# Kernel optimization log

Hardware: AMD Instinct MI355X
Metric: run time of the kernel (lower is better)

## Reference

```python
import jax, jax.numpy as jnp
import numpy as np

B, N, D, L = 8, 2048, 256, 2  # batch, node_size, in_dim==mem_dim, num_layers


def setup_inputs() -> dict:
    key = jax.random.key(0)
    k_nodes, k_adj, k_w0, k_b0, k_wr, k_br = jax.random.split(key, 6)
    nodes = jax.random.normal(k_nodes, (B, N, D), dtype=jnp.float32)
    adj = jax.random.uniform(k_adj, (B, N, N), dtype=jnp.float32)
    s = 1.0 / np.sqrt(D)
    W0_w = jax.random.uniform(k_w0, (L, D, D), dtype=jnp.float32, minval=-s, maxval=s)
    W0_b = jax.random.uniform(k_b0, (L, D), dtype=jnp.float32, minval=-s, maxval=s)
    Wr_w = jax.random.uniform(k_wr, (L, D, D), dtype=jnp.float32, minval=-s, maxval=s)
    Wr_b = jax.random.uniform(k_br, (L, D), dtype=jnp.float32, minval=-s, maxval=s)
    return {"nodes": nodes, "adj": adj, "W0_w": W0_w, "W0_b": W0_b,
            "Wr_w": Wr_w, "Wr_b": Wr_b}


def reference(nodes, adj, W0_w, W0_b, Wr_w, Wr_b):
    # denom[b] = row-sum of adj[b] + 1  -> [B, N, 1]
    denom = jnp.sum(adj, axis=2, keepdims=True) + 1.0
    x = nodes  # dropout is identity in eval mode
    outputs = x
    for l in range(L):
        # W_r branch: aggregate neighbor-transformed features
        xWr = jnp.einsum('bnd,md->bnm', x, Wr_w[l]) + Wr_b[l]   # [B,N,D]
        AxW = jnp.einsum('bnk,bkd->bnd', adj, xWr)              # sparse mm equiv
        # W_0 self branch, fused norm + relu
        xW0 = jnp.einsum('bnd,md->bnm', x, W0_w[l]) + W0_b[l]
        x = jax.nn.relu((AxW + xW0) / denom)
    return outputs + x
```

## Files before the change

### kernel.cpp

```cpp
#include <hip/hip_runtime.h>

constexpr int B = 8;
constexpr int N = 2048;
constexpr int D = 256;
constexpr int L = 2;
constexpr int M = B * N;

typedef __bf16 bf16x8 __attribute__((ext_vector_type(8)));
typedef float  f32x4  __attribute__((ext_vector_type(4)));

static __device__ __forceinline__ unsigned short f2bf(float f) {
    union { float f; unsigned u; } v; v.f = f;
    unsigned r = v.u + 0x7fffu + ((v.u >> 16) & 1u);
    return (unsigned short)(r >> 16);
}

static __device__ __forceinline__ float bf2f(unsigned short u) {
    union { unsigned u; float f; } v; v.u = ((unsigned)u) << 16;
    return v.f;
}

static __device__ __forceinline__ void gload16(const void* g, void* l) {
    __builtin_amdgcn_global_load_lds(
        (__attribute__((address_space(1))) void*)(g),
        (__attribute__((address_space(3))) void*)(l),
        16, 0, 0);
}

__global__ __launch_bounds__(256)
void denom_cast_kernel(const float* __restrict__ adj,
                       unsigned short* __restrict__ adjb,
                       float* __restrict__ rdenom,
                       float* __restrict__ rowsum) {
    const int wave = threadIdx.x >> 6;
    const int lane = threadIdx.x & 63;
    const int row  = blockIdx.x * 4 + wave;
    const float4* p = (const float4*)(adj + (size_t)row * N);
    ushort4* q = (ushort4*)(adjb + (size_t)row * N);
    float s = 0.f;
    #pragma unroll
    for (int i = 0; i < 8; ++i) {
        float4 v = p[lane + i * 64];
        s += (v.x + v.y) + (v.z + v.w);
        ushort4 o;
        o.x = f2bf(v.x); o.y = f2bf(v.y); o.z = f2bf(v.z); o.w = f2bf(v.w);
        q[lane + i * 64] = o;
    }
    #pragma unroll
    for (int off = 32; off > 0; off >>= 1) s += __shfl_down(s, off);
    if (lane == 0) {
        rowsum[row] = s;
        rdenom[row] = 1.0f / (s + 1.0f);
    }
}

__global__ __launch_bounds__(256)
void cast_nodes_kernel(const float* __restrict__ nodes,
                       unsigned short* __restrict__ nodesbf,
                       unsigned short* __restrict__ nodesT) {
    __shared__ unsigned short T[64][68];
    const int b  = blockIdx.z;
    const int n0 = blockIdx.y * 64;
    const int d0 = blockIdx.x * 64;
    const int t  = threadIdx.x;
    const int r  = t >> 2;
    const int c4 = t & 3;
    const float*    src = nodes   + ((size_t)b * N + n0) * D + d0;
    unsigned short* dst = nodesbf + ((size_t)b * N + n0) * D + d0;
    #pragma unroll
    for (int rep = 0; rep < 4; ++rep) {
        const int fc = c4 + rep * 4;
        float4 v = *(const float4*)(src + (size_t)r * D + fc * 4);
        ushort4 o;
        o.x = f2bf(v.x); o.y = f2bf(v.y); o.z = f2bf(v.z); o.w = f2bf(v.w);
        *(ushort4*)(dst + (size_t)r * D + fc * 4) = o;
        *(ushort4*)&T[r][fc * 4] = o;
    }
    __syncthreads();
    unsigned short* dstT = nodesT + ((size_t)b * D + d0) * N + n0;
    #pragma unroll
    for (int rep = 0; rep < 4; ++rep) {
        const int nc = c4 + rep * 4;
        ushort4 o;
        o.x = T[nc * 4 + 0][r];
        o.y = T[nc * 4 + 1][r];
        o.z = T[nc * 4 + 2][r];
        o.w = T[nc * 4 + 3][r];
        *(ushort4*)(dstT + (size_t)r * N + nc * 4) = o;
    }
}

__global__ __launch_bounds__(256)
void cast_w_kernel(const float* __restrict__ W0_w, const float* __restrict__ Wr_w,
                   unsigned short* __restrict__ W0b, unsigned short* __restrict__ Wrb) {
    const int i = blockIdx.x * 256 + threadIdx.x;
    float4 a = ((const float4*)W0_w)[i];
    ushort4 o0; o0.x = f2bf(a.x); o0.y = f2bf(a.y); o0.z = f2bf(a.z); o0.w = f2bf(a.w);
    ((ushort4*)W0b)[i] = o0;
    float4 c = ((const float4*)Wr_w)[i];
    ushort4 o1; o1.x = f2bf(c.x); o1.y = f2bf(c.y); o1.z = f2bf(c.z); o1.w = f2bf(c.w);
    ((ushort4*)Wrb)[i] = o1;
}

__global__ __launch_bounds__(256)
void big_mfma_kernel(const unsigned short* __restrict__ adjb,
                     const unsigned short* __restrict__ xT,
                     unsigned short* __restrict__ ypart) {
    __shared__ unsigned short As[16 * 512];
    __shared__ unsigned short Bs[16 * 512];

    const int z     = blockIdx.z;
    const int b     = z & 7;
    const int split = z >> 3;
    const int n0    = blockIdx.x * 128;
    const int m0    = blockIdx.y * 128;
    const int t     = threadIdx.x;
    const int w     = t >> 6;
    const int lane  = t & 63;
    const int lrow  = lane & 15;
    const int lk    = (lane >> 4) * 8;
    const int kbase = split * (N / 2);

    const unsigned short* Ab = adjb + (size_t)b * N * N + kbase;
    const unsigned short* Bb = xT   + (size_t)b * D * N + kbase;

    const unsigned short* gA0 = Ab + (size_t)(m0 + (2 * w + 0) * 16 + lrow) * N + lk;
    const unsigned short* gA1 = Ab + (size_t)(m0 + (2 * w + 1) * 16 + lrow) * N + lk;
    const unsigned short* gB0 = Bb + (size_t)(n0 + (2 * w + 0) * 16 + lrow) * N + lk;
    const unsigned short* gB1 = Bb + (size_t)(n0 + (2 * w + 1) * 16 + lrow) * N + lk;

    f32x4 acc[4][4];
    const f32x4 zero = {0.f, 0.f, 0.f, 0.f};
    #pragma unroll
    for (int i = 0; i < 4; ++i)
        #pragma unroll
        for (int j = 0; j < 4; ++j) acc[i][j] = zero;

    for (int k0 = 0; k0 < N / 2; k0 += 64) {
        __syncthreads();
        gload16(gA0 + k0,      &As[((2 * w + 0) * 2 + 0) * 512]);
        gload16(gA0 + k0 + 32, &As[((2 * w + 0) * 2 + 1) * 512]);
        gload16(gA1 + k0,      &As[((2 * w + 1) * 2 + 0) * 512]);
        gload16(gA1 + k0 + 32, &As[((2 * w + 1) * 2 + 1) * 512]);
        gload16(gB0 + k0,      &Bs[((2 * w + 0) * 2 + 0) * 512]);
        gload16(gB0 + k0 + 32, &Bs[((2 * w + 0) * 2 + 1) * 512]);
        gload16(gB1 + k0,      &Bs[((2 * w + 1) * 2 + 0) * 512]);
        gload16(gB1 + k0 + 32, &Bs[((2 * w + 1) * 2 + 1) * 512]);
        __syncthreads();
        #pragma unroll
        for (int kc = 0; kc < 2; ++kc) {
            bf16x8 a[4], bb[4];
            #pragma unroll
            for (int i = 0; i < 4; ++i)
                a[i] = *(const bf16x8*)&As[((((w & 1) * 4 + i) * 2) + kc) * 512 + lane * 8];
            #pragma unroll
            for (int j = 0; j < 4; ++j)
                bb[j] = *(const bf16x8*)&Bs[((((w >> 1) * 4 + j) * 2) + kc) * 512 + lane * 8];
            #pragma unroll
            for (int i = 0; i < 4; ++i)
                #pragma unroll
                for (int j = 0; j < 4; ++j)
                    acc[i][j] = __builtin_amdgcn_mfma_f32_16x16x32_bf16(
                        a[i], bb[j], acc[i][j], 0, 0, 0);
        }
    }

    unsigned short* yb = ypart + ((size_t)split * M + (size_t)b * N) * D;
    const int col  = lane & 15;
    const int quad = lane >> 4;
    #pragma unroll
    for (int i = 0; i < 4; ++i) {
        const int mBase = m0 + (w & 1) * 64 + i * 16 + quad * 4;
        #pragma unroll
        for (int r = 0; r < 4; ++r) {
            const size_t rowOff = (size_t)(mBase + r) * D;
            #pragma unroll
            for (int j = 0; j < 4; ++j) {
                const int d = n0 + (w >> 1) * 64 + j * 16 + col;
                yb[rowOff + d] = f2bf(acc[i][j][r]);
            }
        }
    }
}

__global__ __launch_bounds__(256)
void small_mfma_kernel(const unsigned short* __restrict__ y0,
                       const unsigned short* __restrict__ y1,
                       const unsigned short* __restrict__ x,
                       const unsigned short* __restrict__ Wrb,
                       const unsigned short* __restrict__ W0b,
                       const float* __restrict__ br,
                       const float* __restrict__ b0,
                       const float* __restrict__ rdenom,
                       const float* __restrict__ rowsum,
                       const unsigned short* __restrict__ nodesbf,
                       unsigned short* __restrict__ xout,
                       unsigned short* __restrict__ xoutT,
                       float* __restrict__ out) {
    __shared__ unsigned short As[16 * 512];
    __shared__ unsigned short Bs[8 * 512];

    const int n0   = blockIdx.x * 64;
    const int m0   = blockIdx.y * 128;
    const int t    = threadIdx.x;
    const int w    = t >> 6;
    const int lane = t & 63;
    const int lrow = lane & 15;
    const int lk   = (lane >> 4) * 8;

    const size_t aRow0 = (size_t)(m0 + (2 * w + 0) * 16 + lrow) * D + lk;
    const size_t aRow1 = (size_t)(m0 + (2 * w + 1) * 16 + lrow) * D + lk;
    const size_t bRow  = (size_t)(n0 + w * 16 + lrow) * D + lk;

    f32x4 acc[4][2];
    const f32x4 zero = {0.f, 0.f, 0.f, 0.f};
    #pragma unroll
    for (int i = 0; i < 4; ++i)
        #pragma unroll
        for (int j = 0; j < 2; ++j) acc[i][j] = zero;

    #pragma unroll
    for (int s = 0; s < 3; ++s) {
        const unsigned short* Asrc = (s == 0) ? y0 : (s == 1) ? y1 : x;
        const unsigned short* Bsrc = (s < 2) ? Wrb : W0b;
        #pragma unroll
        for (int kk = 0; kk < D; kk += 64) {
            __syncthreads();
            gload16(Asrc + aRow0 + kk,      &As[((2 * w + 0) * 2 + 0) * 512]);
            gload16(Asrc + aRow0 + kk + 32, &As[((2 * w + 0) * 2 + 1) * 512]);
            gload16(Asrc + aRow1 + kk,      &As[((2 * w + 1) * 2 + 0) * 512]);
            gload16(Asrc + aRow1 + kk + 32, &As[((2 * w + 1) * 2 + 1) * 512]);
            gload16(Bsrc + bRow + kk,       &Bs[(w * 2 + 0) * 512]);
            gload16(Bsrc + bRow + kk + 32,  &Bs[(w * 2 + 1) * 512]);
            __syncthreads();
            #pragma unroll
            for (int kc = 0; kc < 2; ++kc) {
                bf16x8 a[4], bb[2];
                #pragma unroll
                for (int i = 0; i < 4; ++i)
                    a[i] = *(const bf16x8*)&As[((((w & 1) * 4 + i) * 2) + kc) * 512 + lane * 8];
                #pragma unroll
                for (int j = 0; j < 2; ++j)
                    bb[j] = *(const bf16x8*)&Bs[((((w >> 1) * 2 + j) * 2) + kc) * 512 + lane * 8];
                #pragma unroll
                for (int i = 0; i < 4; ++i)
                    #pragma unroll
                    for (int j = 0; j < 2; ++j)
                        acc[i][j] = __builtin_amdgcn_mfma_f32_16x16x32_bf16(
                            a[i], bb[j], acc[i][j], 0, 0, 0);
            }
        }
    }

    const int col  = lane & 15;
    const int quad = lane >> 4;
    #pragma unroll
    for (int i = 0; i < 4; ++i) {
        const int mBase = m0 + (w & 1) * 64 + i * 16 + quad * 4;
        float rd[4], ss[4];
        #pragma unroll
        for (int r = 0; r < 4; ++r) {
            rd[r] = rdenom[mBase + r];
            ss[r] = rowsum[mBase + r];
        }
        #pragma unroll
        for (int j = 0; j < 2; ++j) {
            const int jj = n0 + (w >> 1) * 32 + j * 16 + col;
            const float bj = b0[jj];
            const float bv = br[jj];
            if (out) {
                #pragma unroll
                for (int r = 0; r < 4; ++r) {
                    const size_t idx = (size_t)(mBase + r) * D + jj;
                    float v = (acc[i][j][r] + bj + bv * ss[r]) * rd[r];
                    out[idx] = bf2f(nodesbf[idx]) + fmaxf(v, 0.f);
                }
            } else {
                ushort4 o;
                float v0 = fmaxf((acc[i][j][0] + bj + bv * ss[0]) * rd[0], 0.f);
                float v1 = fmaxf((acc[i][j][1] + bj + bv * ss[1]) * rd[1], 0.f);
                float v2 = fmaxf((acc[i][j][2] + bj + bv * ss[2]) * rd[2], 0.f);
                float v3 = fmaxf((acc[i][j][3] + bj + bv * ss[3]) * rd[3], 0.f);
                o.x = f2bf(v0); o.y = f2bf(v1); o.z = f2bf(v2); o.w = f2bf(v3);
                xout[(size_t)(mBase + 0) * D + jj] = o.x;
                xout[(size_t)(mBase + 1) * D + jj] = o.y;
                xout[(size_t)(mBase + 2) * D + jj] = o.z;
                xout[(size_t)(mBase + 3) * D + jj] = o.w;
                const int bb_ = m0 >> 11;
                const int nloc = mBase & (N - 1);
                *(ushort4*)&xoutT[((size_t)bb_ * D + jj) * N + nloc] = o;
            }
        }
    }
}

extern "C" void kernel_launch(void* const* d_in, const int* in_sizes, int n_in,
                              void* d_out, int out_size, void* d_ws, size_t ws_size,
                              hipStream_t stream) {
    const float* nodes = (const float*)d_in[0];
    const float* adj   = (const float*)d_in[1];
    const float* W0_w  = (const float*)d_in[2];
    const float* W0_b  = (const float*)d_in[3];
    const float* Wr_w  = (const float*)d_in[4];
    const float* Wr_b  = (const float*)d_in[5];
    float* out = (float*)d_out;

    unsigned short* adjb    = (unsigned short*)d_ws;
    unsigned short* xTbuf   = adjb  + (size_t)B * N * N;
    unsigned short* nodesbf = xTbuf + (size_t)B * D * N;
    unsigned short* ybuf    = nodesbf + (size_t)B * N * D;
    unsigned short* x1      = ybuf  + (size_t)2 * M * D;
    unsigned short* Wrb     = x1    + (size_t)M * D;
    unsigned short* W0b     = Wrb   + (size_t)L * D * D;
    float* rdenom = (float*)(W0b + (size_t)L * D * D);
    float* rowsum = rdenom + M;

    denom_cast_kernel<<<dim3(B * N / 4), 256, 0, stream>>>(adj, adjb, rdenom, rowsum);
    cast_nodes_kernel<<<dim3(D / 64, N / 64, B), 256, 0, stream>>>(nodes, nodesbf, xTbuf);
    cast_w_kernel<<<dim3(L * D * D / 4 / 256), 256, 0, stream>>>(W0_w, Wr_w, W0b, Wrb);

    unsigned short* y0 = ybuf;
    unsigned short* y1 = ybuf + (size_t)M * D;

    big_mfma_kernel<<<dim3(D / 128, N / 128, 2 * B), 256, 0, stream>>>(adjb, xTbuf, ybuf);
    small_mfma_kernel<<<dim3(D / 64, M / 128), 256, 0, stream>>>(
        y0, y1, nodesbf, Wrb, W0b, Wr_b, W0_b, rdenom, rowsum,
        nullptr, x1, xTbuf, nullptr);

    big_mfma_kernel<<<dim3(D / 128, N / 128, 2 * B), 256, 0, stream>>>(adjb, xTbuf, ybuf);
    small_mfma_kernel<<<dim3(D / 64, M / 128), 256, 0, stream>>>(
        y0, y1, x1, Wrb + D * D, W0b + D * D, Wr_b + D, W0_b + D, rdenom, rowsum,
        nodesbf, nullptr, nullptr, out);
}
```

Measured before the change: 341.5 us.

## Use FP8 adjacency and features in big aggregation GEMM and fuse prep kernels

Quantizes the adjacency matrix and the transposed node features to FP8 e4m3 and switches the N×N aggregation GEMM to the fp8 MFMA. This halves the bytes streamed from memory and into LDS in the dominant kernel. The three prep kernels are merged into one launch, and the final residual now reads the fp32 nodes directly. The trade-off is lower numerical precision in the aggregation: uniform adjacency values and ReLU outputs are quantized to about 3 mantissa bits, which may break the tolerance.

```diff
diff --git a/kernel.cpp b/kernel.cpp
--- a/kernel.cpp
+++ b/kernel.cpp
@@ -1,4 +1,5 @@
 #include <hip/hip_runtime.h>
+#include <hip/hip_fp8.h>
 
 constexpr int B = 8;
 constexpr int N = 2048;
@@ -15,9 +16,9 @@
     return (unsigned short)(r >> 16);
 }
 
-static __device__ __forceinline__ float bf2f(unsigned short u) {
-    union { unsigned u; float f; } v; v.u = ((unsigned)u) << 16;
-    return v.f;
+static __device__ __forceinline__ unsigned char f2fp8(float f) {
+    __hip_fp8_e4m3 v(f);
+    return (unsigned char)v.__x;
 }
 
 static __device__ __forceinline__ void gload16(const void* g, void* l) {
@@ -28,86 +29,88 @@
 }
 
 __global__ __launch_bounds__(256)
-void denom_cast_kernel(const float* __restrict__ adj,
-                       unsigned short* __restrict__ adjb,
-                       float* __restrict__ rdenom,
-                       float* __restrict__ rowsum) {
-    const int wave = threadIdx.x >> 6;
-    const int lane = threadIdx.x & 63;
-    const int row  = blockIdx.x * 4 + wave;
-    const float4* p = (const float4*)(adj + (size_t)row * N);
-    ushort4* q = (ushort4*)(adjb + (size_t)row * N);
-    float s = 0.f;
-    #pragma unroll
-    for (int i = 0; i < 8; ++i) {
-        float4 v = p[lane + i * 64];
-        s += (v.x + v.y) + (v.z + v.w);
-        ushort4 o;
-        o.x = f2bf(v.x); o.y = f2bf(v.y); o.z = f2bf(v.z); o.w = f2bf(v.w);
-        q[lane + i * 64] = o;
-    }
-    #pragma unroll
-    for (int off = 32; off > 0; off >>= 1) s += __shfl_down(s, off);
-    if (lane == 0) {
-        rowsum[row] = s;
-        rdenom[row] = 1.0f / (s + 1.0f);
+void prep_kernel(const float* __restrict__ adj,
+                 const float* __restrict__ nodes,
+                 const float* __restrict__ W0_w, const float* __restrict__ Wr_w,
+                 unsigned char* __restrict__ adj8,
+                 float* __restrict__ rdenom, float* __restrict__ rowsum,
+                 unsigned short* __restrict__ nodesbf,
+                 unsigned char* __restrict__ nodesT8,
+                 unsigned short* __restrict__ W0b, unsigned short* __restrict__ Wrb) {
+    __shared__ unsigned char T8[64][68];
+    const int bx = blockIdx.x;
+    const int t  = threadIdx.x;
+    if (bx < 4096) {
+        const int wave = t >> 6;
+        const int lane = t & 63;
+        const int row  = bx * 4 + wave;
+        const float4* p = (const float4*)(adj + (size_t)row * N);
+        uchar4* q = (uchar4*)(adj8 + (size_t)row * N);
+        float s = 0.f;
+        #pragma unroll
+        for (int i = 0; i < 8; ++i) {
+            float4 v = p[lane + i * 64];
+            s += (v.x + v.y) + (v.z + v.w);
+            uchar4 o;
+            o.x = f2fp8(v.x); o.y = f2fp8(v.y); o.z = f2fp8(v.z); o.w = f2fp8(v.w);
+            q[lane + i * 64] = o;
+        }
+        #pragma unroll
+        for (int off = 32; off > 0; off >>= 1) s += __shfl_down(s, off);
+        if (lane == 0) {
+            rowsum[row] = s;
+            rdenom[row] = 1.0f / (s + 1.0f);
+        }
+    } else if (bx < 4096 + 1024) {
+        const int idx = bx - 4096;
+        const int b   = idx >> 7;
+        const int rem = idx & 127;
+        const int n0  = (rem >> 2) * 64;
+        const int d0  = (rem & 3) * 64;
+        const int r   = t >> 2;
+        const int c4  = t & 3;
+        const float*    src = nodes   + ((size_t)b * N + n0) * D + d0;
+        unsigned short* dst = nodesbf + ((size_t)b * N + n0) * D + d0;
+        #pragma unroll
+        for (int rep = 0; rep < 4; ++rep) {
+            const int fc = c4 + rep * 4;
+            float4 v = *(const float4*)(src + (size_t)r * D + fc * 4);
+            ushort4 o;
+            o.x = f2bf(v.x); o.y = f2bf(v.y); o.z = f2bf(v.z); o.w = f2bf(v.w);
+            *(ushort4*)(dst + (size_t)r * D + fc * 4) = o;
+            uchar4 o8;
+            o8.x = f2fp8(v.x); o8.y = f2fp8(v.y); o8.z = f2fp8(v.z); o8.w = f2fp8(v.w);
+            *(uchar4*)&T8[r][fc * 4] = o8;
+        }
+        __syncthreads();
+        unsigned char* dstT = nodesT8 + ((size_t)b * D + d0) * N + n0;
+        #pragma unroll
+        for (int rep = 0; rep < 4; ++rep) {
+            const int nc = c4 + rep * 4;
+            uchar4 o;
+            o.x = T8[nc * 4 + 0][r];
+            o.y = T8[nc * 4 + 1][r];
+            o.z = T8[nc * 4 + 2][r];
+            o.w = T8[nc * 4 + 3][r];
+            *(uchar4*)(dstT + (size_t)r * N + nc * 4) = o;
+        }
+    } else {
+        const int i = (bx - 5120) * 256 + t;
+        float4 a = ((const float4*)W0_w)[i];
+        ushort4 o0; o0.x = f2bf(a.x); o0.y = f2bf(a.y); o0.z = f2bf(a.z); o0.w = f2bf(a.w);
+        ((ushort4*)W0b)[i] = o0;
+        float4 c = ((const float4*)Wr_w)[i];
+        ushort4 o1; o1.x = f2bf(c.x); o1.y = f2bf(c.y); o1.z = f2bf(c.z); o1.w = f2bf(c.w);
+        ((ushort4*)Wrb)[i] = o1;
     }
 }
 
 __global__ __launch_bounds__(256)
-void cast_nodes_kernel(const float* __restrict__ nodes,
-                       unsigned short* __restrict__ nodesbf,
-                       unsigned short* __restrict__ nodesT) {
-    __shared__ unsigned short T[64][68];
-    const int b  = blockIdx.z;
-    const int n0 = blockIdx.y * 64;
-    const int d0 = blockIdx.x * 64;
-    const int t  = threadIdx.x;
-    const int r  = t >> 2;
-    const int c4 = t & 3;
-    const float*    src = nodes   + ((size_t)b * N + n0) * D + d0;
-    unsigned short* dst = nodesbf + ((size_t)b * N + n0) * D + d0;
-    #pragma unroll
-    for (int rep = 0; rep < 4; ++rep) {
-        const int fc = c4 + rep * 4;
-        float4 v = *(const float4*)(src + (size_t)r * D + fc * 4);
-        ushort4 o;
-        o.x = f2bf(v.x); o.y = f2bf(v.y); o.z = f2bf(v.z); o.w = f2bf(v.w);
-        *(ushort4*)(dst + (size_t)r * D + fc * 4) = o;
-        *(ushort4*)&T[r][fc * 4] = o;
-    }
-    __syncthreads();
-    unsigned short* dstT = nodesT + ((size_t)b * D + d0) * N + n0;
-    #pragma unroll
-    for (int rep = 0; rep < 4; ++rep) {
-        const int nc = c4 + rep * 4;
-        ushort4 o;
-        o.x = T[nc * 4 + 0][r];
-        o.y = T[nc * 4 + 1][r];
-        o.z = T[nc * 4 + 2][r];
-        o.w = T[nc * 4 + 3][r];
-        *(ushort4*)(dstT + (size_t)r * N + nc * 4) = o;
-    }
-}
-
-__global__ __launch_bounds__(256)
-void cast_w_kernel(const float* __restrict__ W0_w, const float* __restrict__ Wr_w,
-                   unsigned short* __restrict__ W0b, unsigned short* __restrict__ Wrb) {
-    const int i = blockIdx.x * 256 + threadIdx.x;
-    float4 a = ((const float4*)W0_w)[i];
-    ushort4 o0; o0.x = f2bf(a.x); o0.y = f2bf(a.y); o0.z = f2bf(a.z); o0.w = f2bf(a.w);
-    ((ushort4*)W0b)[i] = o0;
-    float4 c = ((const float4*)Wr_w)[i];
-    ushort4 o1; o1.x = f2bf(c.x); o1.y = f2bf(c.y); o1.z = f2bf(c.z); o1.w = f2bf(c.w);
-    ((ushort4*)Wrb)[i] = o1;
-}
-
-__global__ __launch_bounds__(256)
-void big_mfma_kernel(const unsigned short* __restrict__ adjb,
-                     const unsigned short* __restrict__ xT,
+void big_mfma_kernel(const unsigned char* __restrict__ adj8,
+                     const unsigned char* __restrict__ xT8,
                      unsigned short* __restrict__ ypart) {
-    __shared__ unsigned short As[16 * 512];
-    __shared__ unsigned short Bs[16 * 512];
+    __shared__ __align__(16) unsigned char As[8 * 1024];
+    __shared__ __align__(16) unsigned char Bs[8 * 1024];
 
     const int z     = blockIdx.z;
     const int b     = z & 7;
@@ -118,16 +121,17 @@
     const int w     = t >> 6;
     const int lane  = t & 63;
     const int lrow  = lane & 15;
-    const int lk    = (lane >> 4) * 8;
+    const int lkc   = (lane >> 4) * 16;
+    const int q     = lane >> 4;
     const int kbase = split * (N / 2);
 
-    const unsigned short* Ab = adjb + (size_t)b * N * N + kbase;
-    const unsigned short* Bb = xT   + (size_t)b * D * N + kbase;
-
-    const unsigned short* gA0 = Ab + (size_t)(m0 + (2 * w + 0) * 16 + lrow) * N + lk;
-    const unsigned short* gA1 = Ab + (size_t)(m0 + (2 * w + 1) * 16 + lrow) * N + lk;
-    const unsigned short* gB0 = Bb + (size_t)(n0 + (2 * w + 0) * 16 + lrow) * N + lk;
-    const unsigned short* gB1 = Bb + (size_t)(n0 + (2 * w + 1) * 16 + lrow) * N + lk;
+    const unsigned char* Ab = adj8 + (size_t)b * N * N + kbase;
+    const unsigned char* Bb = xT8  + (size_t)b * D * N + kbase;
+
+    const unsigned char* gA0 = Ab + (size_t)(m0 + (2 * w + 0) * 16 + lrow) * N + lkc;
+    const unsigned char* gA1 = Ab + (size_t)(m0 + (2 * w + 1) * 16 + lrow) * N + lkc;
+    const unsigned char* gB0 = Bb + (size_t)(n0 + (2 * w + 0) * 16 + lrow) * N + lkc;
+    const unsigned char* gB1 = Bb + (size_t)(n0 + (2 * w + 1) * 16 + lrow) * N + lkc;
 
     f32x4 acc[4][4];
     const f32x4 zero = {0.f, 0.f, 0.f, 0.f};
@@ -138,29 +142,26 @@
 
     for (int k0 = 0; k0 < N / 2; k0 += 64) {
         __syncthreads();
-        gload16(gA0 + k0,      &As[((2 * w + 0) * 2 + 0) * 512]);
-        gload16(gA0 + k0 + 32, &As[((2 * w + 0) * 2 + 1) * 512]);
-        gload16(gA1 + k0,      &As[((2 * w + 1) * 2 + 0) * 512]);
-        gload16(gA1 + k0 + 32, &As[((2 * w + 1) * 2 + 1) * 512]);
-        gload16(gB0 + k0,      &Bs[((2 * w + 0) * 2 + 0) * 512]);
-        gload16(gB0 + k0 + 32, &Bs[((2 * w + 0) * 2 + 1) * 512]);
-        gload16(gB1 + k0,      &Bs[((2 * w + 1) * 2 + 0) * 512]);
-        gload16(gB1 + k0 + 32, &Bs[((2 * w + 1) * 2 + 1) * 512]);
+        gload16(gA0 + k0, &As[(2 * w + 0) * 1024]);
+        gload16(gA1 + k0, &As[(2 * w + 1) * 1024]);
+        gload16(gB0 + k0, &Bs[(2 * w + 0) * 1024]);
+        gload16(gB1 + k0, &Bs[(2 * w + 1) * 1024]);
         __syncthreads();
         #pragma unroll
         for (int kc = 0; kc < 2; ++kc) {
-            bf16x8 a[4], bb[4];
+            const int off = (2 * kc + (q >> 1)) * 256 + lrow * 16 + (q & 1) * 8;
+            long long a[4], bb[4];
             #pragma unroll
             for (int i = 0; i < 4; ++i)
-                a[i] = *(const bf16x8*)&As[((((w & 1) * 4 + i) * 2) + kc) * 512 + lane * 8];
+                a[i] = *(const long long*)&As[((w & 1) * 4 + i) * 1024 + off];
             #pragma unroll
             for (int j = 0; j < 4; ++j)
-                bb[j] = *(const bf16x8*)&Bs[((((w >> 1) * 4 + j) * 2) + kc) * 512 + lane * 8];
+                bb[j] = *(const long long*)&Bs[((w >> 1) * 4 + j) * 1024 + off];
             #pragma unroll
             for (int i = 0; i < 4; ++i)
                 #pragma unroll
                 for (int j = 0; j < 4; ++j)
-                    acc[i][j] = __builtin_amdgcn_mfma_f32_16x16x32_bf16(
+                    acc[i][j] = __builtin_amdgcn_mfma_f32_16x16x32_fp8_fp8(
                         a[i], bb[j], acc[i][j], 0, 0, 0);
         }
     }
@@ -193,12 +194,12 @@
                        const float* __restrict__ b0,
                        const float* __restrict__ rdenom,
                        const float* __restrict__ rowsum,
-                       const unsigned short* __restrict__ nodesbf,
+                       const float* __restrict__ nodesf,
                        unsigned short* __restrict__ xout,
-                       unsigned short* __restrict__ xoutT,
+                       unsigned char* __restrict__ xoutT8,
                        float* __restrict__ out) {
-    __shared__ unsigned short As[16 * 512];
-    __shared__ unsigned short Bs[8 * 512];
+    __shared__ __align__(16) unsigned short As[16 * 512];
+    __shared__ __align__(16) unsigned short Bs[8 * 512];
 
     const int n0   = blockIdx.x * 64;
     const int m0   = blockIdx.y * 128;
@@ -273,22 +274,22 @@
                 for (int r = 0; r < 4; ++r) {
                     const size_t idx = (size_t)(mBase + r) * D + jj;
                     float v = (acc[i][j][r] + bj + bv * ss[r]) * rd[r];
-                    out[idx] = bf2f(nodesbf[idx]) + fmaxf(v, 0.f);
+                    out[idx] = nodesf[idx] + fmaxf(v, 0.f);
                 }
             } else {
-                ushort4 o;
                 float v0 = fmaxf((acc[i][j][0] + bj + bv * ss[0]) * rd[0], 0.f);
                 float v1 = fmaxf((acc[i][j][1] + bj + bv * ss[1]) * rd[1], 0.f);
                 float v2 = fmaxf((acc[i][j][2] + bj + bv * ss[2]) * rd[2], 0.f);
                 float v3 = fmaxf((acc[i][j][3] + bj + bv * ss[3]) * rd[3], 0.f);
-                o.x = f2bf(v0); o.y = f2bf(v1); o.z = f2bf(v2); o.w = f2bf(v3);
-                xout[(size_t)(mBase + 0) * D + jj] = o.x;
-                xout[(size_t)(mBase + 1) * D + jj] = o.y;
-                xout[(size_t)(mBase + 2) * D + jj] = o.z;
-                xout[(size_t)(mBase + 3) * D + jj] = o.w;
-                const int bb_ = m0 >> 11;
+                xout[(size_t)(mBase + 0) * D + jj] = f2bf(v0);
+                xout[(size_t)(mBase + 1) * D + jj] = f2bf(v1);
+                xout[(size_t)(mBase + 2) * D + jj] = f2bf(v2);
+                xout[(size_t)(mBase + 3) * D + jj] = f2bf(v3);
+                uchar4 o8;
+                o8.x = f2fp8(v0); o8.y = f2fp8(v1); o8.z = f2fp8(v2); o8.w = f2fp8(v3);
+                const int bb_  = m0 >> 11;
                 const int nloc = mBase & (N - 1);
-                *(ushort4*)&xoutT[((size_t)bb_ * D + jj) * N + nloc] = o;
+                *(uchar4*)&xoutT8[((size_t)bb_ * D + jj) * N + nloc] = o8;
             }
         }
     }
@@ -305,30 +306,30 @@
     const float* Wr_b  = (const float*)d_in[5];
     float* out = (float*)d_out;
 
-    unsigned short* adjb    = (unsigned short*)d_ws;
-    unsigned short* xTbuf   = adjb  + (size_t)B * N * N;
-    unsigned short* nodesbf = xTbuf + (size_t)B * D * N;
-    unsigned short* ybuf    = nodesbf + (size_t)B * N * D;
-    unsigned short* x1      = ybuf  + (size_t)2 * M * D;
-    unsigned short* Wrb     = x1    + (size_t)M * D;
-    unsigned short* W0b     = Wrb   + (size_t)L * D * D;
+    unsigned char*  adj8    = (unsigned char*)d_ws;
+    unsigned char*  xT8     = adj8 + (size_t)B * N * N;
+    unsigned short* nodesbf = (unsigned short*)(xT8 + (size_t)B * D * N);
+    unsigned short* ybuf    = nodesbf + (size_t)M * D;
+    unsigned short* x1      = ybuf + (size_t)2 * M * D;
+    unsigned short* Wrb     = x1 + (size_t)M * D;
+    unsigned short* W0b     = Wrb + (size_t)L * D * D;
     float* rdenom = (float*)(W0b + (size_t)L * D * D);
     float* rowsum = rdenom + M;
 
-    denom_cast_kernel<<<dim3(B * N / 4), 256, 0, stream>>>(adj, adjb, rdenom, rowsum);
-    cast_nodes_kernel<<<dim3(D / 64, N / 64, B), 256, 0, stream>>>(nodes, nodesbf, xTbuf);
-    cast_w_kernel<<<dim3(L * D * D / 4 / 256), 256, 0, stream>>>(W0_w, Wr_w, W0b, Wrb);
+    prep_kernel<<<dim3(5248), 256, 0, stream>>>(
+        adj, nodes, W0_w, Wr_w,
+        adj8, rdenom, rowsum, nodesbf, xT8, W0b, Wrb);
 
     unsigned short* y0 = ybuf;
     unsigned short* y1 = ybuf + (size_t)M * D;
 
-    big_mfma_kernel<<<dim3(D / 128, N / 128, 2 * B), 256, 0, stream>>>(adjb, xTbuf, ybuf);
+    big_mfma_kernel<<<dim3(D / 128, N / 128, 2 * B), 256, 0, stream>>>(adj8, xT8, ybuf);
     small_mfma_kernel<<<dim3(D / 64, M / 128), 256, 0, stream>>>(
         y0, y1, nodesbf, Wrb, W0b, Wr_b, W0_b, rdenom, rowsum,
-        nullptr, x1, xTbuf, nullptr);
-
-    big_mfma_kernel<<<dim3(D / 128, N / 128, 2 * B), 256, 0, stream>>>(adjb, xTbuf, ybuf);
+        nullptr, x1, xT8, nullptr);
+
+    big_mfma_kernel<<<dim3(D / 128, N / 128, 2 * B), 256, 0, stream>>>(adj8, xT8, ybuf);
     small_mfma_kernel<<<dim3(D / 64, M / 128), 256, 0, stream>>>(
         y0, y1, x1, Wrb + D * D, W0b + D * D, Wr_b + D, W0_b + D, rdenom, rowsum,
-        nodesbf, nullptr, nullptr, out);
-}
+        nodes, nullptr, nullptr, out);
+}
```

Measured after the change: 318.7 us. -6.7%, faster.
